# Optimization experiments

Hardware: AMD Instinct MI355X
Metric: run time of the kernel (lower is better)

Reference implementation:

```python
import jax
import jax.numpy as jnp
from jax import lax
import numpy as np

INPUT_DIM = 784
HIDDEN_DIM = 1024
BATCH = 256
N_BINS = 10


def setup_inputs() -> dict:
    key = jax.random.key(0)
    k1, k2, k3, k4, k5 = jax.random.split(key, 5)
    # kaiming-normal-ish init scales (faithful in spirit; exact values irrelevant for math)
    W = jax.random.normal(k1, (HIDDEN_DIM, INPUT_DIM), dtype=jnp.float32) * np.sqrt(2.0 / INPUT_DIM)
    c = jnp.zeros((HIDDEN_DIM, 1), dtype=jnp.float32)
    V = jax.random.normal(k2, (INPUT_DIM, HIDDEN_DIM, N_BINS), dtype=jnp.float32) * np.sqrt(2.0 / N_BINS)
    b = jnp.zeros((INPUT_DIM, N_BINS), dtype=jnp.float32)
    x = jax.random.randint(k3, (BATCH, INPUT_DIM), 0, N_BINS, dtype=jnp.int32)
    return {"x": x, "W": W, "c": c, "V": V, "b": b}


def reference(x, W, c, V, b):
    # x: [B, D] int pixel bins; W: [H, D]; c: [H, 1]; V: [D, H, 10]; b: [D, 10]
    B = x.shape[0]
    xf = x.astype(jnp.float32)  # [B, D]
    a0 = jnp.broadcast_to(c[:, 0][None, :], (B, W.shape[0]))  # [B, H]

    def step(a, inp):
        Vi, bi, Wi, xi = inp  # Vi:[H,10], bi:[10], Wi:[H], xi:[B]
        h = jax.nn.sigmoid(a)                       # [B, H]
        p = jax.nn.softmax(h @ Vi + bi, axis=1)     # [B, 10]
        a = a + xi[:, None] * Wi[None, :]           # rank-1 update, matches x_i @ W[:,i].T
        return a, p

    _, p_seq = lax.scan(step, a0, (V, b, W.T, xf.T))  # p_seq: [D, B, 10]
    p_hat = jnp.transpose(p_seq, (1, 2, 0))            # [B, 10, D] == torch.stack(p_hat, dim=2)
    return p_hat
```

## Files before the change

kernel.cpp:

```cpp
#include <hip/hip_runtime.h>
#include <stdint.h>

#define D_DIM 784
#define H_DIM 1024
#define B_DIM 256
#define NBIN  10
#define G_CH  8
#define T_CH  98
#define BT    16
#define BF    2
#define LOG2E 1.4426950408889634f

typedef _Float16 half8_t  __attribute__((ext_vector_type(8)));
typedef __fp16   fp16x2_t __attribute__((ext_vector_type(2)));
typedef float    float4_t __attribute__((ext_vector_type(4)));

__global__ void k_prep(const float* __restrict__ W, const float* __restrict__ V,
                       _Float16* __restrict__ Wt2h, _Float16* __restrict__ VB) {
    __shared__ __align__(16) float smem[H_DIM * NBIN];
    int tid = threadIdx.x;
    if (blockIdx.x < D_DIM) {
        int i = blockIdx.x;
        const float4* src = (const float4*)(V + (size_t)i * H_DIM * NBIN);
        #pragma unroll
        for (int q = 0; q < 10; ++q) {
            float4 v = src[q * 256 + tid];
            *((float4*)&smem[(q * 256 + tid) * 4]) = v;
        }
        __syncthreads();
        #pragma unroll
        for (int q = 0; q < 8; ++q) {
            int pair = q * 256 + tid;
            int kk = pair >> 6, l = pair & 63;
            int n = l & 15, hb = kk * 32 + ((l >> 4) & 3) * 8;
            union { _Float16 h[8]; uint4 u; } o;
            #pragma unroll
            for (int jj = 0; jj < 8; ++jj)
                o.h[jj] = (_Float16)((n < NBIN) ? smem[(hb + jj) * NBIN + n] : 0.0f);
            ((uint4*)VB)[(size_t)i * 2048 + pair] = o.u;
        }
    } else {
        int q = blockIdx.x - D_DIM;
        int j0 = (q % 13) * 64, h0 = (q / 13) * 64;
        float (*t)[65] = (float(*)[65])smem;
        int tj = tid & 63, tr = tid >> 6;
        int j = j0 + tj;
        #pragma unroll
        for (int r = 0; r < 16; ++r) {
            int hh = tr * 16 + r;
            t[hh][tj] = (j < D_DIM) ? W[(size_t)(h0 + hh) * D_DIM + j] : 0.0f;
        }
        __syncthreads();
        #pragma unroll
        for (int r = 0; r < 16; ++r) {
            int jj = tr * 16 + r;
            int jo = j0 + jj;
            if (jo < D_DIM) Wt2h[(size_t)jo * H_DIM + h0 + tj] = (_Float16)(t[tj][jj] * LOG2E);
        }
    }
}

__global__ void k_pscan(const _Float16* __restrict__ Wt2h, const int* __restrict__ x,
                        const float* __restrict__ c, _Float16* __restrict__ PA) {
    int b0 = blockIdx.x * BF;
    int h  = blockIdx.y * 256 + threadIdx.x;
    __shared__ float xs[BF][D_DIM];
    for (int q = threadIdx.x; q < BF * (D_DIM / 4); q += 256) {
        int bb = q / (D_DIM / 4), r = q % (D_DIM / 4);
        int4 xi = ((const int4*)(x + (size_t)(b0 + bb) * D_DIM))[r];
        float4 xf = make_float4((float)xi.x, (float)xi.y, (float)xi.z, (float)xi.w);
        *((float4*)&xs[bb][r * 4]) = xf;
    }
    float acc0 = c[h] * LOG2E, acc1 = acc0;
    __syncthreads();
    for (int t = 0; t < T_CH; ++t) {
        PA[((size_t)t * B_DIM + b0 + 0) * H_DIM + h] = (_Float16)acc0;
        PA[((size_t)t * B_DIM + b0 + 1) * H_DIM + h] = (_Float16)acc1;
        #pragma unroll
        for (int j = 0; j < G_CH; ++j) {
            float wv = (float)Wt2h[(size_t)(t * G_CH + j) * H_DIM + h];
            acc0 += xs[0][t * G_CH + j] * wv;
            acc1 += xs[1][t * G_CH + j] * wv;
        }
    }
}

__global__ __launch_bounds__(256, 2)
void k_main(const _Float16* __restrict__ VB, const _Float16* __restrict__ Wt2h,
            const _Float16* __restrict__ PA, const int* __restrict__ x,
            const float* __restrict__ bias, float* __restrict__ out) {
    int bt  = blockIdx.x;
    int tc  = blockIdx.y;
    int tid = threadIdx.x;
    int w   = tid >> 6;
    int l   = tid & 63;
    int bl  = l & 15;
    int kg  = l >> 4;
    int bg  = bt * BT + bl;
    int i0  = tc * G_CH;

    __shared__ __align__(16) _Float16 wlds[G_CH][H_DIM];
    __shared__ float red[4][64][18];
    __shared__ float bs[G_CH][16];

    {
        int ii = tid >> 4, n = tid & 15;
        if (ii < G_CH) bs[ii][n] = (n < NBIN) ? bias[(size_t)(i0 + ii) * NBIN + n] : 0.0f;
    }
    {
        #pragma unroll
        for (int r = 0; r < G_CH; ++r) {
            uint2 v = ((const uint2*)(Wt2h + (size_t)(i0 + r) * H_DIM))[tid];
            *((uint2*)&wlds[r][tid * 4]) = v;
        }
    }
    float xvf[G_CH];
    {
        const int4* xp = (const int4*)(x + (size_t)bg * D_DIM + i0);
        int4 x0 = xp[0], x1 = xp[1];
        xvf[0] = (float)x0.x; xvf[1] = (float)x0.y; xvf[2] = (float)x0.z; xvf[3] = (float)x0.w;
        xvf[4] = (float)x1.x; xvf[5] = (float)x1.y; xvf[6] = (float)x1.z; xvf[7] = (float)x1.w;
    }
    float a[8][8];
    {
        const _Float16* src = PA + ((size_t)tc * B_DIM + bg) * H_DIM + w * 256 + kg * 8;
        #pragma unroll
        for (int m = 0; m < 8; ++m) {
            half8_t av = *((const half8_t*)(src + m * 32));
            #pragma unroll
            for (int j = 0; j < 8; ++j) a[m][j] = (float)av[j];
        }
    }
    __syncthreads();

    const uint4* vbbase = (const uint4*)VB;
    float4_t cf[G_CH];

    auto compute_ii = [&](int ii) {
        int i = i0 + ii;
        uint4 vb[8];
        const uint4* vbp = vbbase + ((size_t)i * 32 + w * 8) * 64 + l;
        #pragma unroll
        for (int m = 0; m < 8; ++m) vb[m] = vbp[m * 64];
        float xf = xvf[ii];
        float4_t cfr = {0.f, 0.f, 0.f, 0.f};
        #pragma unroll
        for (int m = 0; m < 8; ++m) {
            union { half8_t h8; uint u32[4]; } af;
            #pragma unroll
            for (int p = 0; p < 4; ++p) {
                float s0 = __builtin_amdgcn_rcpf(1.0f + __builtin_amdgcn_exp2f(-a[m][2 * p]));
                float s1 = __builtin_amdgcn_rcpf(1.0f + __builtin_amdgcn_exp2f(-a[m][2 * p + 1]));
                union { fp16x2_t v; uint u; } cv;
                cv.v = __builtin_amdgcn_cvt_pkrtz(s0, s1);
                af.u32[p] = cv.u;
            }
            union { half8_t h8; uint4 u; } bf;
            bf.u = vb[m];
            cfr = __builtin_amdgcn_mfma_f32_16x16x32_f16(af.h8, bf.h8, cfr, 0, 0, 0);
            half8_t wh = *((const half8_t*)&wlds[ii][w * 256 + kg * 8 + m * 32]);
            a[m][0] += xf * (float)wh[0]; a[m][1] += xf * (float)wh[1];
            a[m][2] += xf * (float)wh[2]; a[m][3] += xf * (float)wh[3];
            a[m][4] += xf * (float)wh[4]; a[m][5] += xf * (float)wh[5];
            a[m][6] += xf * (float)wh[6]; a[m][7] += xf * (float)wh[7];
        }
        cf[ii] = cfr;
    };

    auto softmax_store = [&](int half) {
        float p4[4];
        #pragma unroll
        for (int q = 0; q < 4; ++q) {
            int ii = half * 4 + q;
            float tot = red[0][l][q * 4 + w] + red[1][l][q * 4 + w]
                      + red[2][l][q * 4 + w] + red[3][l][q * 4 + w];
            float v = (bl < NBIN) ? tot + bs[ii][bl] : -3.0e38f;
            float vm = v;
            vm = fmaxf(vm, __shfl_xor(vm, 1));
            vm = fmaxf(vm, __shfl_xor(vm, 2));
            vm = fmaxf(vm, __shfl_xor(vm, 4));
            vm = fmaxf(vm, __shfl_xor(vm, 8));
            float e = __builtin_amdgcn_exp2f((v - vm) * LOG2E);
            float ss = e;
            ss += __shfl_xor(ss, 1); ss += __shfl_xor(ss, 2);
            ss += __shfl_xor(ss, 4); ss += __shfl_xor(ss, 8);
            p4[q] = e * __builtin_amdgcn_rcpf(ss);
        }
        if (bl < NBIN) {
            int b = bt * BT + kg * 4 + w;
            size_t base = ((size_t)b * NBIN + bl) * D_DIM + i0 + half * 4;
            float4 v = make_float4(p4[0], p4[1], p4[2], p4[3]);
            *((float4*)(out + base)) = v;
        }
    };

    for (int q = 0; q < 4; ++q) compute_ii(q);
    #pragma unroll
    for (int q = 0; q < 4; ++q) {
        #pragma unroll
        for (int r = 0; r < 4; ++r) red[w][l][q * 4 + r] = cf[q][r];
    }
    __syncthreads();
    for (int q = 0; q < 4; ++q) compute_ii(4 + q);
    softmax_store(0);
    __syncthreads();
    #pragma unroll
    for (int q = 0; q < 4; ++q) {
        #pragma unroll
        for (int r = 0; r < 4; ++r) red[w][l][q * 4 + r] = cf[4 + q][r];
    }
    __syncthreads();
    softmax_store(1);
}

extern "C" void kernel_launch(void* const* d_in, const int* in_sizes, int n_in,
                              void* d_out, int out_size, void* d_ws, size_t ws_size,
                              hipStream_t stream) {
    const int*   x    = (const int*)d_in[0];
    const float* W    = (const float*)d_in[1];
    const float* c    = (const float*)d_in[2];
    const float* V    = (const float*)d_in[3];
    const float* bias = (const float*)d_in[4];
    float* out = (float*)d_out;

    char* ws = (char*)d_ws;
    size_t off = 0;
    _Float16* Wt2h = (_Float16*)(ws + off);
    off += (size_t)D_DIM * H_DIM * sizeof(_Float16);
    off = (off + 255) & ~(size_t)255;
    _Float16* VB = (_Float16*)(ws + off);
    off += (size_t)D_DIM * 32 * 64 * 8 * sizeof(_Float16);
    off = (off + 255) & ~(size_t)255;
    _Float16* PA = (_Float16*)(ws + off);

    k_prep<<<dim3(D_DIM + 208), 256, 0, stream>>>(W, V, Wt2h, VB);
    k_pscan<<<dim3(B_DIM / BF, 4), 256, 0, stream>>>(Wt2h, x, c, PA);
    k_main<<<dim3(B_DIM / BT, T_CH), 256, 0, stream>>>(VB, Wt2h, PA, x, bias, out);
}
```

Measured before the change: 191.0 us.

## Fuse prefix scan into prep kernel and software-pipeline V loads in main

Folds the partial-sum scan into the prep kernel as extra blocks that read the original fp32 W directly, so it no longer waits on the transposed fp16 W and one kernel launch disappears. In the main kernel, per-step V fragment loads become a three-slot rotating prefetch two steps ahead, and per-chunk results are written to the reduction buffer right after each chunk, which removes the register array of eight accumulators. Launch bounds are raised to four blocks per CU for more occupancy, at the risk of register spills. The scan now reads W rows with a strided per-thread access pattern, which may coalesce worse.

```diff
diff --git a/kernel.cpp b/kernel.cpp
--- a/kernel.cpp
+++ b/kernel.cpp
@@ -11,37 +11,87 @@
 #define BF    2
 #define LOG2E 1.4426950408889634f
 
+#define PSCAN_BLKS 512
+#define VPREP_BLKS D_DIM
+#define WPREP_BLKS 208
+
 typedef _Float16 half8_t  __attribute__((ext_vector_type(8)));
 typedef __fp16   fp16x2_t __attribute__((ext_vector_type(2)));
 typedef float    float4_t __attribute__((ext_vector_type(4)));
 
-__global__ void k_prep(const float* __restrict__ W, const float* __restrict__ V,
-                       _Float16* __restrict__ Wt2h, _Float16* __restrict__ VB) {
+__global__ void k_prep2(const float* __restrict__ W, const float* __restrict__ V,
+                        const float* __restrict__ c, const int* __restrict__ x,
+                        _Float16* __restrict__ Wt2h, _Float16* __restrict__ VB,
+                        _Float16* __restrict__ PA) {
     __shared__ __align__(16) float smem[H_DIM * NBIN];
     int tid = threadIdx.x;
-    if (blockIdx.x < D_DIM) {
-        int i = blockIdx.x;
+    int bx  = blockIdx.x;
+
+    if (bx < PSCAN_BLKS) {
+        int q  = bx;
+        int b0 = (q & 127) * BF;
+        int h  = (q >> 7) * 256 + tid;
+        float* xs0 = smem;
+        float* xs1 = smem + D_DIM;
+        for (int qq = tid; qq < BF * (D_DIM / 4); qq += 256) {
+            int bb = qq / (D_DIM / 4), r = qq % (D_DIM / 4);
+            int4 xi = ((const int4*)(x + (size_t)(b0 + bb) * D_DIM))[r];
+            float4 xf = make_float4((float)xi.x, (float)xi.y, (float)xi.z, (float)xi.w);
+            *((float4*)((bb ? xs1 : xs0) + r * 4)) = xf;
+        }
+        float acc0 = c[h], acc1 = acc0;
+        __syncthreads();
+        const float4* w4 = (const float4*)(W + (size_t)h * D_DIM);
+        _Float16* pa = PA + (size_t)b0 * H_DIM + h;
+
+        auto pstore = [&](int t_) {
+            pa[(size_t)t_ * (B_DIM * H_DIM)]         = (_Float16)(acc0 * LOG2E);
+            pa[(size_t)t_ * (B_DIM * H_DIM) + H_DIM] = (_Float16)(acc1 * LOG2E);
+        };
+        auto pfma = [&](float4 w0_, float4 w1_, int t_) {
+            float4 xa0 = *((const float4*)(xs0 + t_ * 8));
+            float4 xa1 = *((const float4*)(xs0 + t_ * 8 + 4));
+            float4 xb0 = *((const float4*)(xs1 + t_ * 8));
+            float4 xb1 = *((const float4*)(xs1 + t_ * 8 + 4));
+            acc0 += xa0.x*w0_.x + xa0.y*w0_.y + xa0.z*w0_.z + xa0.w*w0_.w
+                  + xa1.x*w1_.x + xa1.y*w1_.y + xa1.z*w1_.z + xa1.w*w1_.w;
+            acc1 += xb0.x*w0_.x + xb0.y*w0_.y + xb0.z*w0_.z + xb0.w*w0_.w
+                  + xb1.x*w1_.x + xb1.y*w1_.y + xb1.z*w1_.z + xb1.w*w1_.w;
+        };
+
+        float4 wA0 = w4[0], wA1 = w4[1], wB0 = w4[2], wB1 = w4[3];
+        for (int t = 0; t < T_CH - 2; t += 2) {
+            float4 nA0 = w4[(t + 2) * 2], nA1 = w4[(t + 2) * 2 + 1];
+            float4 nB0 = w4[(t + 3) * 2], nB1 = w4[(t + 3) * 2 + 1];
+            pstore(t);     pfma(wA0, wA1, t);
+            pstore(t + 1); pfma(wB0, wB1, t + 1);
+            wA0 = nA0; wA1 = nA1; wB0 = nB0; wB1 = nB1;
+        }
+        pstore(96); pfma(wA0, wA1, 96);
+        pstore(97);
+    } else if (bx < PSCAN_BLKS + VPREP_BLKS) {
+        int i = bx - PSCAN_BLKS;
         const float4* src = (const float4*)(V + (size_t)i * H_DIM * NBIN);
         #pragma unroll
-        for (int q = 0; q < 10; ++q) {
-            float4 v = src[q * 256 + tid];
-            *((float4*)&smem[(q * 256 + tid) * 4]) = v;
+        for (int qv = 0; qv < 10; ++qv) {
+            float4 v = src[qv * 256 + tid];
+            *((float4*)&smem[(qv * 256 + tid) * 4]) = v;
         }
         __syncthreads();
         #pragma unroll
-        for (int q = 0; q < 8; ++q) {
-            int pair = q * 256 + tid;
-            int kk = pair >> 6, l = pair & 63;
-            int n = l & 15, hb = kk * 32 + ((l >> 4) & 3) * 8;
-            union { _Float16 h[8]; uint4 u; } o;
+        for (int qv = 0; qv < 8; ++qv) {
+            int pair = qv * 256 + tid;
+            int kk = pair >> 6, ll = pair & 63;
+            int n = ll & 15, hb = kk * 32 + ((ll >> 4) & 3) * 8;
+            union { _Float16 hh[8]; uint4 u; } o;
             #pragma unroll
             for (int jj = 0; jj < 8; ++jj)
-                o.h[jj] = (_Float16)((n < NBIN) ? smem[(hb + jj) * NBIN + n] : 0.0f);
+                o.hh[jj] = (_Float16)((n < NBIN) ? smem[(hb + jj) * NBIN + n] : 0.0f);
             ((uint4*)VB)[(size_t)i * 2048 + pair] = o.u;
         }
     } else {
-        int q = blockIdx.x - D_DIM;
-        int j0 = (q % 13) * 64, h0 = (q / 13) * 64;
+        int qw = bx - PSCAN_BLKS - VPREP_BLKS;
+        int j0 = (qw % 13) * 64, h0 = (qw / 13) * 64;
         float (*t)[65] = (float(*)[65])smem;
         int tj = tid & 63, tr = tid >> 6;
         int j = j0 + tj;
@@ -60,32 +110,7 @@
     }
 }
 
-__global__ void k_pscan(const _Float16* __restrict__ Wt2h, const int* __restrict__ x,
-                        const float* __restrict__ c, _Float16* __restrict__ PA) {
-    int b0 = blockIdx.x * BF;
-    int h  = blockIdx.y * 256 + threadIdx.x;
-    __shared__ float xs[BF][D_DIM];
-    for (int q = threadIdx.x; q < BF * (D_DIM / 4); q += 256) {
-        int bb = q / (D_DIM / 4), r = q % (D_DIM / 4);
-        int4 xi = ((const int4*)(x + (size_t)(b0 + bb) * D_DIM))[r];
-        float4 xf = make_float4((float)xi.x, (float)xi.y, (float)xi.z, (float)xi.w);
-        *((float4*)&xs[bb][r * 4]) = xf;
-    }
-    float acc0 = c[h] * LOG2E, acc1 = acc0;
-    __syncthreads();
-    for (int t = 0; t < T_CH; ++t) {
-        PA[((size_t)t * B_DIM + b0 + 0) * H_DIM + h] = (_Float16)acc0;
-        PA[((size_t)t * B_DIM + b0 + 1) * H_DIM + h] = (_Float16)acc1;
-        #pragma unroll
-        for (int j = 0; j < G_CH; ++j) {
-            float wv = (float)Wt2h[(size_t)(t * G_CH + j) * H_DIM + h];
-            acc0 += xs[0][t * G_CH + j] * wv;
-            acc1 += xs[1][t * G_CH + j] * wv;
-        }
-    }
-}
-
-__global__ __launch_bounds__(256, 2)
+__global__ __launch_bounds__(256, 4)
 void k_main(const _Float16* __restrict__ VB, const _Float16* __restrict__ Wt2h,
             const _Float16* __restrict__ PA, const int* __restrict__ x,
             const float* __restrict__ bias, float* __restrict__ out) {
@@ -131,40 +156,43 @@
             for (int j = 0; j < 8; ++j) a[m][j] = (float)av[j];
         }
     }
-    __syncthreads();
-
-    const uint4* vbbase = (const uint4*)VB;
-    float4_t cf[G_CH];
-
-    auto compute_ii = [&](int ii) {
-        int i = i0 + ii;
-        uint4 vb[8];
-        const uint4* vbp = vbbase + ((size_t)i * 32 + w * 8) * 64 + l;
-        #pragma unroll
-        for (int m = 0; m < 8; ++m) vb[m] = vbp[m * 64];
+
+    const uint4* vp = (const uint4*)VB + ((size_t)i0 * 32 + w * 8) * 64 + l;
+    uint4 vbuf[3];
+    vbuf[0] = vp[0];
+    vbuf[1] = vp[64];
+    float4_t acc = {0.f, 0.f, 0.f, 0.f};
+
+    auto step = [&](int mm) {
+        const int ii = mm >> 3, m = mm & 7;
+        if (mm + 2 < 64) {
+            const int nn = mm + 2;
+            vbuf[nn % 3] = vp[((nn >> 3) * 32 + (nn & 7)) * 64];
+        }
+        union { half8_t h8; uint u32[4]; } af;
+        #pragma unroll
+        for (int p = 0; p < 4; ++p) {
+            float s0 = __builtin_amdgcn_rcpf(1.0f + __builtin_amdgcn_exp2f(-a[m][2 * p]));
+            float s1 = __builtin_amdgcn_rcpf(1.0f + __builtin_amdgcn_exp2f(-a[m][2 * p + 1]));
+            union { fp16x2_t v; uint u; } cv;
+            cv.v = __builtin_amdgcn_cvt_pkrtz(s0, s1);
+            af.u32[p] = cv.u;
+        }
+        union { half8_t h8; uint4 u; } bf;
+        bf.u = vbuf[mm % 3];
+        acc = __builtin_amdgcn_mfma_f32_16x16x32_f16(af.h8, bf.h8, acc, 0, 0, 0);
+        half8_t wh = *((const half8_t*)&wlds[ii][w * 256 + kg * 8 + m * 32]);
         float xf = xvf[ii];
-        float4_t cfr = {0.f, 0.f, 0.f, 0.f};
-        #pragma unroll
-        for (int m = 0; m < 8; ++m) {
-            union { half8_t h8; uint u32[4]; } af;
-            #pragma unroll
-            for (int p = 0; p < 4; ++p) {
-                float s0 = __builtin_amdgcn_rcpf(1.0f + __builtin_amdgcn_exp2f(-a[m][2 * p]));
-                float s1 = __builtin_amdgcn_rcpf(1.0f + __builtin_amdgcn_exp2f(-a[m][2 * p + 1]));
-                union { fp16x2_t v; uint u; } cv;
-                cv.v = __builtin_amdgcn_cvt_pkrtz(s0, s1);
-                af.u32[p] = cv.u;
-            }
-            union { half8_t h8; uint4 u; } bf;
-            bf.u = vb[m];
-            cfr = __builtin_amdgcn_mfma_f32_16x16x32_f16(af.h8, bf.h8, cfr, 0, 0, 0);
-            half8_t wh = *((const half8_t*)&wlds[ii][w * 256 + kg * 8 + m * 32]);
-            a[m][0] += xf * (float)wh[0]; a[m][1] += xf * (float)wh[1];
-            a[m][2] += xf * (float)wh[2]; a[m][3] += xf * (float)wh[3];
-            a[m][4] += xf * (float)wh[4]; a[m][5] += xf * (float)wh[5];
-            a[m][6] += xf * (float)wh[6]; a[m][7] += xf * (float)wh[7];
-        }
-        cf[ii] = cfr;
+        a[m][0] += xf * (float)wh[0]; a[m][1] += xf * (float)wh[1];
+        a[m][2] += xf * (float)wh[2]; a[m][3] += xf * (float)wh[3];
+        a[m][4] += xf * (float)wh[4]; a[m][5] += xf * (float)wh[5];
+        a[m][6] += xf * (float)wh[6]; a[m][7] += xf * (float)wh[7];
+        if (m == 7) {
+            int s = (ii & 3) * 4;
+            red[w][l][s + 0] = acc[0]; red[w][l][s + 1] = acc[1];
+            red[w][l][s + 2] = acc[2]; red[w][l][s + 3] = acc[3];
+            acc = (float4_t){0.f, 0.f, 0.f, 0.f};
+        }
     };
 
     auto softmax_store = [&](int half) {
@@ -194,21 +222,14 @@
         }
     };
 
-    for (int q = 0; q < 4; ++q) compute_ii(q);
+    __syncthreads();
     #pragma unroll
-    for (int q = 0; q < 4; ++q) {
-        #pragma unroll
-        for (int r = 0; r < 4; ++r) red[w][l][q * 4 + r] = cf[q][r];
-    }
-    __syncthreads();
-    for (int q = 0; q < 4; ++q) compute_ii(4 + q);
+    for (int mm = 0; mm < 32; ++mm) step(mm);
+    __syncthreads();
     softmax_store(0);
     __syncthreads();
     #pragma unroll
-    for (int q = 0; q < 4; ++q) {
-        #pragma unroll
-        for (int r = 0; r < 4; ++r) red[w][l][q * 4 + r] = cf[4 + q][r];
-    }
+    for (int mm = 32; mm < 64; ++mm) step(mm);
     __syncthreads();
     softmax_store(1);
 }
@@ -233,7 +254,6 @@
     off = (off + 255) & ~(size_t)255;
     _Float16* PA = (_Float16*)(ws + off);
 
-    k_prep<<<dim3(D_DIM + 208), 256, 0, stream>>>(W, V, Wt2h, VB);
-    k_pscan<<<dim3(B_DIM / BF, 4), 256, 0, stream>>>(Wt2h, x, c, PA);
+    k_prep2<<<dim3(PSCAN_BLKS + VPREP_BLKS + WPREP_BLKS), 256, 0, stream>>>(W, V, c, x, Wt2h, VB, PA);
     k_main<<<dim3(B_DIM / BT, T_CH), 256, 0, stream>>>(VB, Wt2h, PA, x, bias, out);
 }
```

Result: slower. 218.9 us (+14.6%).
